# Optimization experiments

Measured on AMD Instinct MI355X. Metric: run time of the kernel, lower is better.

The kernel has to match this reference:

```python
import jax, jax.numpy as jnp
import numpy as np

D_MODEL = 1024
NUM_HEADS = 16
HEAD_DIM = D_MODEL // NUM_HEADS
SCALE = 1.0 / (HEAD_DIM ** 0.5)


def setup_inputs() -> dict:
    key = jax.random.key(0)
    ks = jax.random.split(key, 5)
    std = 1.0 / np.sqrt(D_MODEL)
    x = jax.random.normal(ks[0], (2, 2048, D_MODEL), dtype=jnp.float32)
    Wq = jax.random.normal(ks[1], (D_MODEL, D_MODEL), dtype=jnp.float32) * std
    Wk = jax.random.normal(ks[2], (D_MODEL, D_MODEL), dtype=jnp.float32) * std
    Wv = jax.random.normal(ks[3], (D_MODEL, D_MODEL), dtype=jnp.float32) * std
    Wo = jax.random.normal(ks[4], (D_MODEL, D_MODEL), dtype=jnp.float32) * std
    zeros = jnp.zeros((D_MODEL,), dtype=jnp.float32)
    return {"x": x, "Wq": Wq, "bq": zeros, "Wk": Wk, "bk": zeros,
            "Wv": Wv, "bv": zeros, "Wo": Wo, "bo": zeros}


def reference(x, Wq, bq, Wk, bk, Wv, bv, Wo, bo):
    B, S, D = x.shape
    H, hd = NUM_HEADS, HEAD_DIM
    # Linear projections (torch Linear: y = x @ W.T + b)
    q = (x @ Wq.T + bq).reshape(B, S, H, hd).transpose(0, 2, 1, 3)  # [B,H,S,hd]
    k = (x @ Wk.T + bk).reshape(B, S, H, hd).transpose(0, 2, 1, 3)
    v = (x @ Wv.T + bv).reshape(B, S, H, hd).transpose(0, 2, 1, 3)
    scores = jnp.einsum('bhqd,bhkd->bhqk', q, k) * SCALE  # [B,H,S,S]
    causal = jnp.tril(jnp.ones((S, S), dtype=bool))
    scores = jnp.where(causal, scores, -jnp.inf)
    attn = jax.nn.softmax(scores, axis=-1)
    out = jnp.einsum('bhqk,bhkd->bhqd', attn, v)  # [B,H,S,hd]
    out = out.transpose(0, 2, 1, 3).reshape(B, S, D)
    return out @ Wo.T + bo
```

## Files before the change

kernel.cpp:

```cpp
#include <hip/hip_runtime.h>
#include <hip/hip_bf16.h>


typedef __attribute__((ext_vector_type(8))) short short8;
typedef __attribute__((ext_vector_type(4))) float f32x4;
typedef __attribute__((ext_vector_type(8))) unsigned short u16x8;
typedef __attribute__((ext_vector_type(4))) unsigned short u16x4;

#define QSCALE 0.1803368801111244f
#define MFMA16(a, b, c) __builtin_amdgcn_mfma_f32_16x16x32_bf16(a, b, c, 0, 0, 0)

__device__ __forceinline__ unsigned short f2bf(float f) {
  unsigned int u = __float_as_uint(f);
  u += 0x7fffu + ((u >> 16) & 1u);
  return (unsigned short)(u >> 16);
}

__device__ __forceinline__ void gload_lds16(const void* g, void* l) {
  __builtin_amdgcn_global_load_lds(
      (const __attribute__((address_space(1))) unsigned int*)g,
      (__attribute__((address_space(3))) unsigned int*)l, 16, 0, 0);
}

__global__ __launch_bounds__(256) void convert_all_kernel(
    const float* __restrict__ x, const float* __restrict__ wq,
    const float* __restrict__ wk, const float* __restrict__ wv,
    const float* __restrict__ wo, unsigned short* __restrict__ xb,
    unsigned short* __restrict__ wqkv, unsigned short* __restrict__ wob) {
  const int b = blockIdx.x, tid = threadIdx.x;
  const float* src;
  unsigned short* dst;
  int i;
  if (b < 4096) { src = x; dst = xb; i = b * 256 + tid; }
  else {
    const int r = b - 4096, seg = r >> 10;
    i = (r & 1023) * 256 + tid;
    src = seg == 0 ? wq : (seg == 1 ? wk : (seg == 2 ? wv : wo));
    dst = seg == 3 ? wob : wqkv + (size_t)seg * 1048576;
  }
  float4 v = ((const float4*)src)[i];
  u16x4 o = {f2bf(v.x), f2bf(v.y), f2bf(v.z), f2bf(v.w)};
  *(u16x4*)(dst + (size_t)i * 4) = o;
}

__global__ __launch_bounds__(512, 2) void gemm_qkv_kernel(
    const unsigned short* __restrict__ xb, const unsigned short* __restrict__ wqkv,
    const float* __restrict__ bq, const float* __restrict__ bk, const float* __restrict__ bv,
    unsigned short* __restrict__ Qb, unsigned short* __restrict__ Kb,
    unsigned short* __restrict__ VTb) {
  __shared__ unsigned short As[3 * 256 * 32];
  __shared__ unsigned short Bs[3 * 256 * 32];

  const int tid = threadIdx.x;
  const int w = tid >> 6, l = tid & 63;
  const int wm = w >> 2, wn = w & 3;
  const int rl = l & 15, hi = l >> 4;

  const int wg = (blockIdx.x & 7) * 24 + (blockIdx.x >> 3);
  const int bm = wg / 12, bn = wg % 12;
  const int tm = bm * 256, tn = bn * 256;

  const unsigned short* Ag = xb + (size_t)(tm + (tid >> 2)) * 1024 + (tid & 3) * 8;
  const unsigned short* Bg = wqkv + (size_t)(tn + (tid >> 2)) * 1024 + (tid & 3) * 8;
  const int wst = w * 512;

#define QKV_STAGE(slot, k0)                                                    \
  {                                                                            \
    gload_lds16(Ag + (k0), As + (slot) * 8192 + wst);                          \
    gload_lds16(Ag + 128 * 1024 + (k0), As + (slot) * 8192 + 4096 + wst);      \
    gload_lds16(Bg + (k0), Bs + (slot) * 8192 + wst);                          \
    gload_lds16(Bg + 128 * 1024 + (k0), Bs + (slot) * 8192 + 4096 + wst);      \
  }

  f32x4 acc[8][4] = {};

  QKV_STAGE(0, 0)
  QKV_STAGE(1, 32)
  asm volatile("s_waitcnt vmcnt(4)" ::: "memory");
  __builtin_amdgcn_s_barrier();
  asm volatile("" ::: "memory");

  const int abase = (wm * 128 + rl) * 32 + hi * 8;
  const int bbase = (wn * 64 + rl) * 32 + hi * 8;

  int sl = 0, sn = 2;
  for (int t = 0; t < 32; ++t) {
    if (t < 30) QKV_STAGE(sn, (t + 2) * 32)

    const unsigned short* Ap = As + sl * 8192;
    const unsigned short* Bp = Bs + sl * 8192;
    short8 bfr[4];
#pragma unroll
    for (int n = 0; n < 4; ++n) bfr[n] = *(const short8*)&Bp[bbase + n * 512];
    short8 afr[8];
#pragma unroll
    for (int m = 0; m < 8; ++m) afr[m] = *(const short8*)&Ap[abase + m * 512];
#pragma unroll
    for (int m = 0; m < 8; ++m)
#pragma unroll
      for (int n = 0; n < 4; ++n)
        acc[m][n] = MFMA16(afr[m], bfr[n], acc[m][n]);

    if (t < 30) asm volatile("s_waitcnt vmcnt(4)" ::: "memory");
    else        asm volatile("s_waitcnt vmcnt(0)" ::: "memory");
    __builtin_amdgcn_s_barrier();
    asm volatile("" ::: "memory");
    sl = (sl == 2) ? 0 : sl + 1;
    sn = (sn == 2) ? 0 : sn + 1;
  }
#undef QKV_STAGE

  const int proj = tn >> 10;
  const float* bias = proj == 0 ? bq : (proj == 1 ? bk : bv);
#pragma unroll
  for (int m = 0; m < 8; ++m) {
    const int row0 = tm + wm * 128 + m * 16 + hi * 4;
    const int b2 = row0 >> 11, s2 = row0 & 2047;
#pragma unroll
    for (int n = 0; n < 4; ++n) {
      const int col = (tn & 1023) + wn * 64 + n * 16 + rl;
      const int h = col >> 6, d = col & 63;
      const float bi = bias[col];
      if (proj == 2) {
        u16x4 pv = {f2bf(acc[m][n][0] + bi), f2bf(acc[m][n][1] + bi),
                    f2bf(acc[m][n][2] + bi), f2bf(acc[m][n][3] + bi)};
        *(u16x4*)&VTb[((size_t)((b2 * 16 + h) * 64 + d)) * 2048 + s2] = pv;
      } else {
        const float sc = (proj == 0) ? QSCALE : 1.0f;
        unsigned short* dst = (proj == 0) ? Qb : Kb;
#pragma unroll
        for (int i = 0; i < 4; ++i)
          dst[((size_t)(b2 * 16 + h) * 2048 + (s2 + i)) * 64 + d] =
              f2bf((acc[m][n][i] + bi) * sc);
      }
    }
  }
}

template<int NF>
__device__ __forceinline__ void gemm_db_mainloop(
    const unsigned short* __restrict__ A, const unsigned short* __restrict__ B,
    int tm, int tn, unsigned short* As0, unsigned short* Bs0,
    f32x4 (&acc)[4][NF]) {
  constexpr int BN = NF * 32;
  const int tid = threadIdx.x;
  const int w = tid >> 6, l = tid & 63;
  const int wr = (w >> 1) * 64, wc = (w & 1) * (BN / 2);
  const int srow = l >> 2;
  const int schunk = (l & 3) * 8;
  const int rl = l & 15, kl = (l >> 4) * 8;
  const int K = 1024;
  unsigned short* As1 = As0 + 128 * 32;
  unsigned short* Bs1 = Bs0 + BN * 32;

#define STAGE_TILE(AP, BP, KOFF)                                               \
  {                                                                            \
    _Pragma("unroll") for (int c = 0; c < 2; ++c) {                            \
      const int rowb = w * 32 + c * 16;                                        \
      gload_lds16(A + (size_t)(tm + rowb + srow) * K + (KOFF) + schunk,        \
                  (AP) + rowb * 32);                                           \
    }                                                                          \
    _Pragma("unroll") for (int c = 0; c < BN / 64; ++c) {                      \
      const int rowb = w * (BN / 4) + c * 16;                                  \
      gload_lds16(B + (size_t)(tn + rowb + srow) * K + (KOFF) + schunk,        \
                  (BP) + rowb * 32);                                           \
    }                                                                          \
  }

  STAGE_TILE(As0, Bs0, 0)
  __syncthreads();
  int p = 0;
  for (int k0 = 0; k0 < K; k0 += 32) {
    unsigned short* Ac = p ? As1 : As0;
    unsigned short* Bc = p ? Bs1 : Bs0;
    if (k0 + 32 < K) {
      unsigned short* An = p ? As0 : As1;
      unsigned short* Bn = p ? Bs0 : Bs1;
      STAGE_TILE(An, Bn, k0 + 32)
    }
    short8 af[4], bf[NF];
#pragma unroll
    for (int m = 0; m < 4; ++m) af[m] = *(const short8*)&Ac[(wr + m * 16 + rl) * 32 + kl];
#pragma unroll
    for (int n = 0; n < NF; ++n) bf[n] = *(const short8*)&Bc[(wc + n * 16 + rl) * 32 + kl];
#pragma unroll
    for (int m = 0; m < 4; ++m)
#pragma unroll
      for (int n = 0; n < NF; ++n)
        acc[m][n] = MFMA16(af[m], bf[n], acc[m][n]);
    __syncthreads();
    p ^= 1;
  }
#undef STAGE_TILE
}

template<bool DIAG>
__device__ __forceinline__ void softmax_pack(
    const f32x4 s[4], float& l_i, char* ps,
    int rl, int hi, int swz, int qrow, int kv0) {
  float p[4][4];
  float rs = 0.f;
#pragma unroll
  for (int f = 0; f < 4; ++f)
#pragma unroll
    for (int i = 0; i < 4; ++i) {
      float sv = s[f][i];
      if (DIAG) sv = (kv0 + f * 16 + hi * 4 + i <= qrow) ? sv : -1e30f;
      const float e = __builtin_amdgcn_exp2f(sv);
      p[f][i] = e;
      rs += e;
    }
  rs += __shfl_xor(rs, 16, 64);
  rs += __shfl_xor(rs, 32, 64);
  l_i += rs;
#pragma unroll
  for (int f = 0; f < 4; ++f) {
    u16x4 pv = {f2bf(p[f][0]), f2bf(p[f][1]), f2bf(p[f][2]), f2bf(p[f][3])};
    *(u16x4*)(ps + rl * 128 + ((f * 32 + hi * 8) ^ swz)) = pv;
  }
}

template<bool L_ON, bool L_DIAG, bool H_DIAG>
__device__ __forceinline__ void attn_stage(
    const char* kb, const char* vb, char* psH, char* psL,
    const short8 qfH[2], const short8 qfL[2],
    f32x4 oH[4], f32x4 oL[4], float& lH, float& lL,
    int rl, int hi, int swz, int qrH, int qrL, int kv0, int w) {
  const int fvH = H_DIAG ? (w + 1) : 4;
  f32x4 sH[4] = {}, sL[4] = {};
  __builtin_amdgcn_s_setprio(1);
#pragma unroll
  for (int f = 0; f < 4; ++f) {
    if (H_DIAG && f >= fvH) continue;
    const char* rowp = kb + (f * 16 + rl) * 128;
#pragma unroll
    for (int kc = 0; kc < 2; ++kc) {
      short8 kf = *(const short8*)(rowp + ((kc * 64 + hi * 16) ^ swz));
      sH[f] = MFMA16(kf, qfH[kc], sH[f]);
      if (L_ON && (!L_DIAG || f < w + 1)) sL[f] = MFMA16(kf, qfL[kc], sL[f]);
    }
  }
  __builtin_amdgcn_s_setprio(0);
  softmax_pack<H_DIAG>(sH, lH, psH, rl, hi, swz, qrH, kv0);
  if (L_ON) softmax_pack<L_DIAG>(sL, lL, psL, rl, hi, swz, qrL, kv0);

  const int kcvH = H_DIAG ? ((w >= 2) ? 2 : 1) : 2;
  const int kcvL = (L_ON && L_DIAG) ? ((w >= 2) ? 2 : 1) : 2;
  __builtin_amdgcn_s_setprio(1);
#pragma unroll
  for (int kc = 0; kc < 2; ++kc) {
    if (H_DIAG && kc >= kcvH) continue;
    short8 paH = *(const short8*)(psH + rl * 128 + ((kc * 64 + hi * 16) ^ swz));
    const bool lpv = L_ON && kc < kcvL;
    short8 paL = {};
    if (lpv) paL = *(const short8*)(psL + rl * 128 + ((kc * 64 + hi * 16) ^ swz));
#pragma unroll
    for (int fd = 0; fd < 4; ++fd) {
      short8 vf = *(const short8*)(vb + (fd * 16 + rl) * 128 + ((kc * 64 + hi * 16) ^ swz));
      oH[fd] = MFMA16(vf, paH, oH[fd]);
      if (lpv) oL[fd] = MFMA16(vf, paL, oL[fd]);
    }
  }
  __builtin_amdgcn_s_setprio(0);
}

__global__ __launch_bounds__(256) void flash_kernel(
    const unsigned short* __restrict__ Q, const unsigned short* __restrict__ K,
    const unsigned short* __restrict__ VT, unsigned short* __restrict__ AO) {
  __shared__ unsigned short KbS[2][64 * 64];
  __shared__ unsigned short VbS[2][64 * 64];
  __shared__ unsigned short PsS[4][2][16 * 64];

  const int tid = threadIdx.x;
  const int w = tid >> 6, l = tid & 63;
  const int rl = l & 15, hi = l >> 4;
  const int swz = (rl & 7) << 4;
  const int bid = blockIdx.x;
  const int g = bid & 7, r = bid >> 3;
  const int bh = g * 4 + (r & 3);
  const int pr = r >> 2;
  const int qtH = 31 - pr, qtL = pr;
  const size_t head_off = (size_t)bh * 2048 * 64;

  const int qrH = qtH * 64 + w * 16 + rl;
  const int qrL = qtL * 64 + w * 16 + rl;

  short8 qfH[2], qfL[2];
  {
    const unsigned short* qp = Q + head_off + (size_t)qrH * 64 + hi * 8;
    qfH[0] = *(const short8*)qp;
    qfH[1] = *(const short8*)(qp + 32);
    qp = Q + head_off + (size_t)qrL * 64 + hi * 8;
    qfL[0] = *(const short8*)qp;
    qfL[1] = *(const short8*)(qp + 32);
  }

  f32x4 oH[4] = {}, oL[4] = {};
  float lH = 0.f, lL = 0.f;

  const int sr = tid >> 2;
  const int swzW = (sr & 7) << 4;
  const int cb0 = (tid & 3) * 32;
  const int kwoff0 = sr * 128 + (cb0 ^ swzW);
  const int kwoff1 = sr * 128 + ((cb0 + 16) ^ swzW);
  const unsigned short* kbase = K + head_off + (size_t)sr * 64 + (tid & 3) * 16;
  const unsigned short* vbase = VT + ((size_t)(bh * 64 + sr)) * 2048 + (tid & 3) * 16;

  u16x8 kra = *(const u16x8*)kbase;
  u16x8 krb = *(const u16x8*)(kbase + 8);
  u16x8 vra = *(const u16x8*)vbase;
  u16x8 vrb = *(const u16x8*)(vbase + 8);
  {
    char* kd = (char*)KbS;
    char* vd = (char*)VbS;
    *(u16x8*)(kd + kwoff0) = kra;
    *(u16x8*)(kd + kwoff1) = krb;
    *(u16x8*)(vd + kwoff0) = vra;
    *(u16x8*)(vd + kwoff1) = vrb;
  }
  kra = *(const u16x8*)(kbase + 4096);
  krb = *(const u16x8*)(kbase + 4096 + 8);
  vra = *(const u16x8*)(vbase + 64);
  vrb = *(const u16x8*)(vbase + 64 + 8);
  __syncthreads();

  char* psH = (char*)&PsS[w][0][0];
  char* psL = (char*)&PsS[w][1][0];

  for (int t = 0; t <= qtH; ++t) {
    const int cur = t & 1;
    const char* kb = (const char*)KbS + cur * 8192;
    const char* vb = (const char*)VbS + cur * 8192;
    const int kv0 = t * 64;

    if (t < qtL)
      attn_stage<true, false, false>(kb, vb, psH, psL, qfH, qfL, oH, oL, lH, lL,
                                     rl, hi, swz, qrH, qrL, kv0, w);
    else if (t == qtL)
      attn_stage<true, true, false>(kb, vb, psH, psL, qfH, qfL, oH, oL, lH, lL,
                                    rl, hi, swz, qrH, qrL, kv0, w);
    else if (t < qtH)
      attn_stage<false, false, false>(kb, vb, psH, psL, qfH, qfL, oH, oL, lH, lL,
                                      rl, hi, swz, qrH, qrL, kv0, w);
    else
      attn_stage<false, false, true>(kb, vb, psH, psL, qfH, qfL, oH, oL, lH, lL,
                                     rl, hi, swz, qrH, qrL, kv0, w);

    if (t < qtH) {
      char* kd = (char*)KbS + (cur ^ 1) * 8192;
      char* vd = (char*)VbS + (cur ^ 1) * 8192;
      *(u16x8*)(kd + kwoff0) = kra;
      *(u16x8*)(kd + kwoff1) = krb;
      *(u16x8*)(vd + kwoff0) = vra;
      *(u16x8*)(vd + kwoff1) = vrb;
      if (t + 2 <= qtH) {
        const size_t ko = (size_t)(t + 2) * 4096;
        kra = *(const u16x8*)(kbase + ko);
        krb = *(const u16x8*)(kbase + ko + 8);
        vra = *(const u16x8*)(vbase + (t + 2) * 64);
        vrb = *(const u16x8*)(vbase + (t + 2) * 64 + 8);
      }
    }
    __syncthreads();
  }

  const float invH = 1.f / lH, invL = 1.f / lL;
  const size_t orowH = (size_t)(bh >> 4) * 2048 + qrH;
  const size_t orowL = (size_t)(bh >> 4) * 2048 + qrL;
  const int hcol = (bh & 15) * 64;
#pragma unroll
  for (int fd = 0; fd < 4; ++fd) {
    u16x4 a = {f2bf(oH[fd][0] * invH), f2bf(oH[fd][1] * invH),
               f2bf(oH[fd][2] * invH), f2bf(oH[fd][3] * invH)};
    *(u16x4*)&AO[orowH * 1024 + hcol + fd * 16 + hi * 4] = a;
    u16x4 b = {f2bf(oL[fd][0] * invL), f2bf(oL[fd][1] * invL),
               f2bf(oL[fd][2] * invL), f2bf(oL[fd][3] * invL)};
    *(u16x4*)&AO[orowL * 1024 + hcol + fd * 16 + hi * 4] = b;
  }
}

__global__ __launch_bounds__(256) void gemm_out_kernel(
    const unsigned short* __restrict__ AOb, const unsigned short* __restrict__ wob,
    const float* __restrict__ bo, float* __restrict__ out) {
  __shared__ unsigned short As[2 * 128 * 32], Bs[2 * 64 * 32];
  f32x4 acc[4][2] = {};
  const int flat = blockIdx.x;
  const int xcd = flat & 7, loc = flat >> 3;
  const int bn = xcd * 2 + (loc & 1), bm = loc >> 1;
  const int tm = bm * 128, tn = bn * 64;
  gemm_db_mainloop<2>(AOb, wob, tm, tn, As, Bs, acc);
  const int tid = threadIdx.x, w = tid >> 6, l = tid & 63;
  const int wr = (w >> 1) * 64, wc = (w & 1) * 32;
  const int rl = l & 15, hi = l >> 4;
#pragma unroll
  for (int m = 0; m < 4; ++m) {
    const int row0 = tm + wr + m * 16 + hi * 4;
#pragma unroll
    for (int n = 0; n < 2; ++n) {
      const int col = tn + wc + n * 16 + rl;
      const float bo_ = bo[col];
#pragma unroll
      for (int i = 0; i < 4; ++i)
        out[(size_t)(row0 + i) * 1024 + col] = acc[m][n][i] + bo_;
    }
  }
}

extern "C" void kernel_launch(void* const* d_in, const int* in_sizes, int n_in,
                              void* d_out, int out_size, void* d_ws, size_t ws_size,
                              hipStream_t stream) {
  const float* x  = (const float*)d_in[0];
  const float* Wq = (const float*)d_in[1];
  const float* bq = (const float*)d_in[2];
  const float* Wk = (const float*)d_in[3];
  const float* bk = (const float*)d_in[4];
  const float* Wv = (const float*)d_in[5];
  const float* bv = (const float*)d_in[6];
  const float* Wo = (const float*)d_in[7];
  const float* bo = (const float*)d_in[8];
  float* out = (float*)d_out;

  unsigned short* ws = (unsigned short*)d_ws;
  unsigned short* XB   = ws;
  unsigned short* WQKV = ws + 4194304;
  unsigned short* WOB  = ws + 7340032;
  unsigned short* QB   = ws + 8388608;
  unsigned short* KB   = ws + 12582912;
  unsigned short* VTB  = ws + 16777216;
  unsigned short* AOB  = XB;

  convert_all_kernel<<<8192, 256, 0, stream>>>(x, Wq, Wk, Wv, Wo, XB, WQKV, WOB);
  gemm_qkv_kernel<<<192, 512, 0, stream>>>(XB, WQKV, bq, bk, bv, QB, KB, VTB);
  flash_kernel<<<512, 256, 0, stream>>>(QB, KB, VTB, AOB);
  gemm_out_kernel<<<512, 256, 0, stream>>>(AOB, WOB, bo, out);
}
```

Before: 197.4 us.

## Split QKV GEMM k-step into two ping-pong phases with priority and barriers

The QKV projection GEMM main loop now runs each k-step in two halves. Global-to-LDS loads are split between them (A loads before the first half, B loads before the second), and each half loads only four A fragments before issuing 16 MFMAs. Extra workgroup barriers, sched_barrier and s_setprio bracket the MFMA clusters so waves alternate between memory and math phases, aiming to overlap loads with compute. This adds barrier overhead and reduces A-fragment register pressure, but whether the interleaving actually hides latency is uncertain.

Result: no change. 198.0 us (+0.3%).

```diff
diff --git a/kernel.cpp b/kernel.cpp
--- a/kernel.cpp
+++ b/kernel.cpp
@@ -64,18 +64,18 @@
   const unsigned short* Bg = wqkv + (size_t)(tn + (tid >> 2)) * 1024 + (tid & 3) * 8;
   const int wst = w * 512;
 
-#define QKV_STAGE(slot, k0)                                                    \
-  {                                                                            \
-    gload_lds16(Ag + (k0), As + (slot) * 8192 + wst);                          \
-    gload_lds16(Ag + 128 * 1024 + (k0), As + (slot) * 8192 + 4096 + wst);      \
-    gload_lds16(Bg + (k0), Bs + (slot) * 8192 + wst);                          \
-    gload_lds16(Bg + 128 * 1024 + (k0), Bs + (slot) * 8192 + 4096 + wst);      \
-  }
-
   f32x4 acc[8][4] = {};
 
-  QKV_STAGE(0, 0)
-  QKV_STAGE(1, 32)
+  {
+    gload_lds16(Ag, As + wst);
+    gload_lds16(Ag + 128 * 1024, As + 4096 + wst);
+    gload_lds16(Bg, Bs + wst);
+    gload_lds16(Bg + 128 * 1024, Bs + 4096 + wst);
+    gload_lds16(Ag + 32, As + 8192 + wst);
+    gload_lds16(Ag + 128 * 1024 + 32, As + 8192 + 4096 + wst);
+    gload_lds16(Bg + 32, Bs + 8192 + wst);
+    gload_lds16(Bg + 128 * 1024 + 32, Bs + 8192 + 4096 + wst);
+  }
   asm volatile("s_waitcnt vmcnt(4)" ::: "memory");
   __builtin_amdgcn_s_barrier();
   asm volatile("" ::: "memory");
@@ -85,30 +85,55 @@
 
   int sl = 0, sn = 2;
   for (int t = 0; t < 32; ++t) {
-    if (t < 30) QKV_STAGE(sn, (t + 2) * 32)
-
     const unsigned short* Ap = As + sl * 8192;
     const unsigned short* Bp = Bs + sl * 8192;
-    short8 bfr[4];
+
+    if (t < 30) {
+      const int k0 = (t + 2) * 32;
+      gload_lds16(Ag + k0, As + sn * 8192 + wst);
+      gload_lds16(Ag + 128 * 1024 + k0, As + sn * 8192 + 4096 + wst);
+    }
+    short8 bfr[4], afr[4];
 #pragma unroll
     for (int n = 0; n < 4; ++n) bfr[n] = *(const short8*)&Bp[bbase + n * 512];
-    short8 afr[8];
-#pragma unroll
-    for (int m = 0; m < 8; ++m) afr[m] = *(const short8*)&Ap[abase + m * 512];
-#pragma unroll
-    for (int m = 0; m < 8; ++m)
+#pragma unroll
+    for (int m = 0; m < 4; ++m) afr[m] = *(const short8*)&Ap[abase + m * 512];
+    __builtin_amdgcn_s_barrier();
+    asm volatile("s_waitcnt lgkmcnt(0)" ::: "memory");
+    __builtin_amdgcn_sched_barrier(0);
+    __builtin_amdgcn_s_setprio(1);
+#pragma unroll
+    for (int m = 0; m < 4; ++m)
 #pragma unroll
       for (int n = 0; n < 4; ++n)
         acc[m][n] = MFMA16(afr[m], bfr[n], acc[m][n]);
-
+    __builtin_amdgcn_s_setprio(0);
+    __builtin_amdgcn_s_barrier();
+
+    if (t < 30) {
+      const int k0 = (t + 2) * 32;
+      gload_lds16(Bg + k0, Bs + sn * 8192 + wst);
+      gload_lds16(Bg + 128 * 1024 + k0, Bs + sn * 8192 + 4096 + wst);
+    }
+    short8 afr2[4];
+#pragma unroll
+    for (int m = 0; m < 4; ++m) afr2[m] = *(const short8*)&Ap[abase + (m + 4) * 512];
+    __builtin_amdgcn_s_barrier();
+    asm volatile("s_waitcnt lgkmcnt(0)" ::: "memory");
+    __builtin_amdgcn_sched_barrier(0);
+    __builtin_amdgcn_s_setprio(1);
+#pragma unroll
+    for (int m = 0; m < 4; ++m)
+#pragma unroll
+      for (int n = 0; n < 4; ++n)
+        acc[m + 4][n] = MFMA16(afr2[m], bfr[n], acc[m + 4][n]);
+    __builtin_amdgcn_s_setprio(0);
     if (t < 30) asm volatile("s_waitcnt vmcnt(4)" ::: "memory");
     else        asm volatile("s_waitcnt vmcnt(0)" ::: "memory");
     __builtin_amdgcn_s_barrier();
-    asm volatile("" ::: "memory");
     sl = (sl == 2) ? 0 : sl + 1;
     sn = (sn == 2) ? 0 : sn + 1;
   }
-#undef QKV_STAGE
 
   const int proj = tn >> 10;
   const float* bias = proj == 0 ? bq : (proj == 1 ? bk : bv);
```
